# Kernel tuning notes

Hardware: AMD Instinct MI355X
Metric: run time of the kernel (lower is better)

The kernel has to match this reference:

```python
import jax, jax.numpy as jnp
import numpy as np

D_MODEL = 1024
NUM_HEADS = 16
D_K = D_MODEL // NUM_HEADS
ROPE_BASE = 10000.0


def _rope_cos_sin(seq_len, d_k):
    inv_freq = 1.0 / (ROPE_BASE ** (jnp.arange(0, d_k, 2, dtype=jnp.float32) / d_k))
    t = jnp.arange(seq_len, dtype=jnp.float32)
    freqs = t[:, None] * inv_freq[None, :]          # [S, d_k/2]
    emb = jnp.concatenate([freqs, freqs], axis=-1)  # [S, d_k]
    return jnp.cos(emb), jnp.sin(emb)


def _rotate_half(x):
    x1, x2 = jnp.split(x, 2, axis=-1)
    return jnp.concatenate([-x2, x1], axis=-1)


def setup_inputs() -> dict:
    key = jax.random.key(0)
    ks = jax.random.split(key, 11)
    B, S, D = 4, 2048, D_MODEL
    scale = 1.0 / np.sqrt(D)
    inp = {
        "query": jax.random.normal(ks[0], (B, S, D), jnp.float32),
        "key": jax.random.normal(ks[1], (B, S, D), jnp.float32),
        "value": jax.random.normal(ks[2], (B, S, D), jnp.float32),
        "W_q": jax.random.normal(ks[3], (D, D), jnp.float32) * scale,
        "b_q": jnp.zeros((D,), jnp.float32),
        "W_k": jax.random.normal(ks[4], (D, D), jnp.float32) * scale,
        "b_k": jnp.zeros((D,), jnp.float32),
        "W_v": jax.random.normal(ks[5], (D, D), jnp.float32) * scale,
        "b_v": jnp.zeros((D,), jnp.float32),
        "W_o": jax.random.normal(ks[6], (D, D), jnp.float32) * scale,
        "b_o": jnp.zeros((D,), jnp.float32),
    }
    return inp


def reference(query, key, value, W_q, b_q, W_k, b_k, W_v, b_v, W_o, b_o):
    B, Sq, D = query.shape
    Sk = key.shape[1]
    H, dk = NUM_HEADS, D_K

    # QKV projections -> [B, H, S, dk]
    Q = (query @ W_q.T + b_q).reshape(B, Sq, H, dk).transpose(0, 2, 1, 3)
    K = (key @ W_k.T + b_k).reshape(B, Sk, H, dk).transpose(0, 2, 1, 3)
    V = (value @ W_v.T + b_v).reshape(B, Sk, H, dk).transpose(0, 2, 1, 3)

    # RoPE
    cos, sin = _rope_cos_sin(Sq, dk)  # [S, dk]
    cos = cos[None, None]
    sin = sin[None, None]
    Q = Q * cos + _rotate_half(Q) * sin
    K = K * cos + _rotate_half(K) * sin

    scores = jnp.einsum("bhqd,bhkd->bhqk", Q, K) / np.sqrt(dk)
    causal_mask = jnp.triu(jnp.ones((Sq, Sk), bool), k=1)
    scores = jnp.where(causal_mask[None, None], -jnp.inf, scores)
    attn = jax.nn.softmax(scores, axis=-1)
    context = jnp.einsum("bhqk,bhkd->bhqd", attn, V)
    context = context.transpose(0, 2, 1, 3).reshape(B, Sq, D)
    return context @ W_o.T + b_o
```

## Files before the change

kernel.cpp:

```cpp
#include <hip/hip_runtime.h>
#include <hip/hip_bf16.h>
#include <cstdint>
#include <cstddef>


typedef __attribute__((ext_vector_type(8))) short short8;
typedef __attribute__((ext_vector_type(4))) float f32x4;
typedef unsigned short u16;

#define LOG2E 1.44269504088896340736f
#define SCALE_Q 0.18033688011112042f

__device__ __forceinline__ u16 f2bf(float f) {
  __hip_bfloat16 h = __float2bfloat16(f);
  return *reinterpret_cast<u16*>(&h);
}
__device__ __forceinline__ float bf2f(short bits) {
  unsigned int u = ((unsigned int)(u16)bits) << 16;
  return __uint_as_float(u);
}
__device__ __forceinline__ void gload_lds16(const void* g, void* l) {
  __builtin_amdgcn_global_load_lds(
      (const __attribute__((address_space(1))) void*)g,
      (__attribute__((address_space(3))) void*)l, 16, 0, 0);
}
__device__ __forceinline__ f32x4 max4(f32x4 a, f32x4 b) {
  f32x4 r;
  r[0] = fmaxf(a[0], b[0]); r[1] = fmaxf(a[1], b[1]);
  r[2] = fmaxf(a[2], b[2]); r[3] = fmaxf(a[3], b[3]);
  return r;
}

__global__ void cvt_f32_to_bf16(const float* __restrict__ in, u16* __restrict__ out, int n4) {
  const int stride = gridDim.x * blockDim.x;
  for (int i = blockIdx.x * blockDim.x + threadIdx.x; i < n4; i += stride) {
    const float4 v = ((const float4*)in)[i];
    ushort4 o;
    o.x = f2bf(v.x); o.y = f2bf(v.y); o.z = f2bf(v.z); o.w = f2bf(v.w);
    ((ushort4*)out)[i] = o;
  }
}

__global__ void rope_tables(float* __restrict__ cost, float* __restrict__ sint, int S) {
  const int idx = blockIdx.x * blockDim.x + threadIdx.x;
  if (idx >= S * 32) return;
  const int s = idx >> 5, i = idx & 31;
  const float invf = powf(10000.0f, -(float)i * (1.0f / 32.0f));
  const float ang = (float)s * invf;
  cost[idx] = cosf(ang);
  sint[idx] = sinf(ang);
}

template<int OUT_F32>
__global__ __launch_bounds__(256, 2)
void gemm_bt(const u16* __restrict__ A, const u16* __restrict__ Bt,
             const float* __restrict__ bias, void* __restrict__ Cout,
             int M, int N, int K) {
  __shared__ u16 As[128 * 64];
  __shared__ u16 Bs[128 * 64];
  const int tid = threadIdx.x;
  const int wid = tid >> 6;
  const int lane = tid & 63;
  const int g = lane >> 4, c = lane & 15;
  const int m0 = blockIdx.x * 128;
  const int n0 = blockIdx.y * 128;
  const int wr = wid >> 1, wc = wid & 1;

  f32x4 acc[4][4];
#pragma unroll
  for (int i = 0; i < 4; ++i)
#pragma unroll
    for (int j = 0; j < 4; ++j) acc[i][j] = (f32x4)(0.0f);

  const int kIters = K >> 6;
  for (int kt = 0; kt < kIters; ++kt) {
    const int k0 = kt << 6;
#pragma unroll
    for (int i = 0; i < 4; ++i) {
      const int chunk = i * 256 + tid;
      const int row = chunk >> 3;
      const int scz = (chunk & 7) ^ (row & 7);
      gload_lds16(A + (size_t)(m0 + row) * K + (k0 + scz * 8),
                  (char*)As + (size_t)(i * 256 + (wid << 6)) * 16);
      gload_lds16(Bt + (size_t)(n0 + row) * K + (k0 + scz * 8),
                  (char*)Bs + (size_t)(i * 256 + (wid << 6)) * 16);
    }
    __syncthreads();
#pragma unroll
    for (int ks = 0; ks < 2; ++ks) {
      short8 af[4], bfr[4];
#pragma unroll
      for (int mi = 0; mi < 4; ++mi) {
        const int row = wr * 64 + mi * 16 + c;
        const int cch = (g + ks * 4) ^ (row & 7);
        af[mi] = *(const short8*)((const char*)As + row * 128 + cch * 16);
      }
#pragma unroll
      for (int ni = 0; ni < 4; ++ni) {
        const int row = wc * 64 + ni * 16 + c;
        const int cch = (g + ks * 4) ^ (row & 7);
        bfr[ni] = *(const short8*)((const char*)Bs + row * 128 + cch * 16);
      }
#pragma unroll
      for (int mi = 0; mi < 4; ++mi)
#pragma unroll
        for (int ni = 0; ni < 4; ++ni)
          acc[mi][ni] = __builtin_amdgcn_mfma_f32_16x16x32_bf16(af[mi], bfr[ni], acc[mi][ni], 0, 0, 0);
    }
    __syncthreads();
  }

  float bv[4];
#pragma unroll
  for (int ni = 0; ni < 4; ++ni) bv[ni] = bias[n0 + wc * 64 + ni * 16 + c];

#pragma unroll
  for (int mi = 0; mi < 4; ++mi)
#pragma unroll
    for (int ni = 0; ni < 4; ++ni)
#pragma unroll
      for (int r = 0; r < 4; ++r) {
        const int row = m0 + wr * 64 + mi * 16 + g * 4 + r;
        const int col = n0 + wc * 64 + ni * 16 + c;
        const float v = acc[mi][ni][r] + bv[ni];
        if (OUT_F32) ((float*)Cout)[(size_t)row * N + col] = v;
        else         ((u16*)Cout)[(size_t)row * N + col] = f2bf(v);
      }
}

__global__ void reshape_rope(const u16* __restrict__ qp, const u16* __restrict__ kp,
                             const u16* __restrict__ vp,
                             const float* __restrict__ cost, const float* __restrict__ sint,
                             u16* __restrict__ Qh, u16* __restrict__ Kh, u16* __restrict__ Vtr,
                             int B, int H, int S) {
  __shared__ u16 tile[64][66];
  const int mode = blockIdx.z;
  const int bh = blockIdx.y;
  const int b = bh / H, h = bh % H;
  const int s0 = blockIdx.x * 64;
  const int t = threadIdx.x;
  const int D = H * 64;

  if (mode < 2) {
    const u16* src = mode ? kp : qp;
    u16* dst = mode ? Kh : Qh;
    const float qs = mode ? 1.0f : SCALE_Q;
    const int s = s0 + (t >> 2);
    const int dc = (t & 3) * 8;
    const u16* pr = src + (size_t)(b * S + s) * D + h * 64;
    const short8 lo = *(const short8*)(pr + dc);
    const short8 hi = *(const short8*)(pr + dc + 32);
    short8 olo, ohi;
#pragma unroll
    for (int j = 0; j < 8; ++j) {
      const float co = cost[s * 32 + dc + j];
      const float si = sint[s * 32 + dc + j];
      const float x1 = bf2f(lo[j]);
      const float x2 = bf2f(hi[j]);
      olo[j] = (short)f2bf((x1 * co - x2 * si) * qs);
      ohi[j] = (short)f2bf((x2 * co + x1 * si) * qs);
    }
    u16* op = dst + ((size_t)bh * S + s) * 64;
    *(short8*)(op + dc) = olo;
    *(short8*)(op + dc + 32) = ohi;
  } else {
#pragma unroll
    for (int it = 0; it < 2; ++it) {
      const int chunk = it * 256 + t;
      const int s = chunk >> 3;
      const int dc = (chunk & 7) * 8;
      const short8 v = *(const short8*)(vp + (size_t)(b * S + s0 + s) * D + h * 64 + dc);
#pragma unroll
      for (int u = 0; u < 8; ++u) tile[s][dc + u] = (u16)v[u];
    }
    __syncthreads();
    const int d = t >> 2;
    const int sc = (t & 3) * 16;
    u16* op = Vtr + ((size_t)bh * 64 + d) * S + s0 + sc;
    short8 v0, v1;
#pragma unroll
    for (int j = 0; j < 8; ++j) v0[j] = (short)tile[sc + j][d];
#pragma unroll
    for (int j = 0; j < 8; ++j) v1[j] = (short)tile[sc + 8 + j][d];
    *(short8*)op = v0;
    *(short8*)(op + 8) = v1;
  }
}

__global__ __launch_bounds__(256, 3)
void attn_kernel(const u16* __restrict__ Qh, const u16* __restrict__ Kh,
                 const u16* __restrict__ Vt, u16* __restrict__ ctx,
                 int B, int H, int S) {
  __shared__ u16 KV[2][2][64 * 64];
  __shared__ u16 Ps[4][16 * 64];
  const int tid = threadIdx.x, wid = tid >> 6, lane = tid & 63;
  const int g = lane >> 4, c = lane & 15;

  const int nstH = gridDim.x;
  const int nwg = nstH * gridDim.y;
  const int lin = blockIdx.x + nstH * blockIdx.y;
  const int tt = (lin & 7) * (nwg >> 3) + (lin >> 3);
  const int bx = tt % nstH;
  const int bh = tt / nstH;
  const int b = bh / H, h = bh % H;
  const int D = H * 64;
  const int NST = nstH * 2;

  const size_t baseQK = (size_t)bh * S * 64;
  const size_t baseV  = (size_t)bh * 64 * S;

  for (int ph = 0; ph < 2; ++ph) {
    const int stile = ph ? (NST - 1 - bx) : bx;
    const int q0 = stile * 128;
    const int KT = (q0 >> 6) + 2;
    const int q0w = q0 + wid * 32;
    const int ktl = (q0w + 31) >> 6;
    const int qg0 = q0w + c, qg1 = q0w + 16 + c;

    short8 qB[2][2];
#pragma unroll
    for (int qf = 0; qf < 2; ++qf)
#pragma unroll
      for (int ks = 0; ks < 2; ++ks)
        qB[qf][ks] = *(const short8*)(Qh + baseQK +
                       (size_t)(q0w + qf * 16 + c) * 64 + ks * 32 + g * 8);

    float m_r[2], l_r[2];
    m_r[0] = m_r[1] = -__builtin_inff();
    l_r[0] = l_r[1] = 0.0f;
    f32x4 o[4][2];
#pragma unroll
    for (int df = 0; df < 4; ++df) { o[df][0] = (f32x4)(0.0f); o[df][1] = (f32x4)(0.0f); }

    auto stage = [&](int buf, int kt) {
#pragma unroll
      for (int i = 0; i < 2; ++i) {
        const int chunk = i * 256 + tid;
        const int row = chunk >> 3;
        const int scz = (chunk & 7) ^ (row & 7);
        gload_lds16(Kh + baseQK + (size_t)(kt * 64 + row) * 64 + scz * 8,
                    (char*)&KV[buf][0][0] + (size_t)(i * 256 + (wid << 6)) * 16);
        gload_lds16(Vt + baseV + (size_t)row * S + (kt * 64 + scz * 8),
                    (char*)&KV[buf][1][0] + (size_t)(i * 256 + (wid << 6)) * 16);
      }
    };

    stage(0, 0);
    __syncthreads();
    int cur = 0;
    for (int kt = 0; kt < KT; ++kt) {
      if (kt + 1 < KT) stage(cur ^ 1, kt + 1);
      if (kt <= ktl) {
        const char* Kb = (const char*)&KV[cur][0][0];
        const char* Vb = (const char*)&KV[cur][1][0];

        f32x4 sc[4][2];
#pragma unroll
        for (int kf = 0; kf < 4; ++kf) { sc[kf][0] = (f32x4)(0.0f); sc[kf][1] = (f32x4)(0.0f); }
#pragma unroll
        for (int ks = 0; ks < 2; ++ks) {
          short8 kA[4];
#pragma unroll
          for (int kf = 0; kf < 4; ++kf) {
            const int row = kf * 16 + c;
            kA[kf] = *(const short8*)(Kb + row * 128 + (((g + 4 * ks) ^ (row & 7))) * 16);
          }
#pragma unroll
          for (int kf = 0; kf < 4; ++kf) {
            sc[kf][0] = __builtin_amdgcn_mfma_f32_16x16x32_bf16(kA[kf], qB[0][ks], sc[kf][0], 0, 0, 0);
            sc[kf][1] = __builtin_amdgcn_mfma_f32_16x16x32_bf16(kA[kf], qB[1][ks], sc[kf][1], 0, 0, 0);
          }
        }

        if (kt == ktl) {
#pragma unroll
          for (int kf = 0; kf < 4; ++kf)
#pragma unroll
            for (int r = 0; r < 4; ++r) {
              const int kg = kt * 64 + kf * 16 + 4 * g + r;
              if (kg > qg0) sc[kf][0][r] = -__builtin_inff();
              if (kg > qg1) sc[kf][1][r] = -__builtin_inff();
            }
        }

        u16* Pw = &Ps[wid][0];
        short8 pB[2][2];
#pragma unroll
        for (int qf = 0; qf < 2; ++qf) {
          f32x4 mm = max4(max4(sc[0][qf], sc[1][qf]), max4(sc[2][qf], sc[3][qf]));
          float pm = fmaxf(fmaxf(mm[0], mm[1]), fmaxf(mm[2], mm[3]));
          pm = fmaxf(pm, __shfl_xor(pm, 16));
          pm = fmaxf(pm, __shfl_xor(pm, 32));
          if (__any(pm > m_r[qf] + 8.0f)) {
            const float mn = fmaxf(m_r[qf], pm);
            const float rs = __builtin_exp2f(m_r[qf] - mn);
            m_r[qf] = mn; l_r[qf] *= rs;
#pragma unroll
            for (int df = 0; df < 4; ++df) o[df][qf] *= rs;
          }
          f32x4 ps4 = (f32x4)(0.0f);
#pragma unroll
          for (int kf = 0; kf < 4; ++kf) {
            f32x4 pv;
#pragma unroll
            for (int r = 0; r < 4; ++r) pv[r] = __builtin_exp2f(sc[kf][qf][r] - m_r[qf]);
            sc[kf][qf] = pv;
            ps4 += pv;
          }
          float psum = (ps4[0] + ps4[1]) + (ps4[2] + ps4[3]);
          psum += __shfl_xor(psum, 16);
          psum += __shfl_xor(psum, 32);
          l_r[qf] += psum;

#pragma unroll
          for (int kf = 0; kf < 4; ++kf) {
            ushort4 pk;
            pk.x = f2bf(sc[kf][qf][0]); pk.y = f2bf(sc[kf][qf][1]);
            pk.z = f2bf(sc[kf][qf][2]); pk.w = f2bf(sc[kf][qf][3]);
            *(ushort4*)((char*)Pw + c * 128 +
                        (((2 * kf + (g >> 1)) ^ (c & 7))) * 16 + 8 * (g & 1)) = pk;
          }
#pragma unroll
          for (int ks = 0; ks < 2; ++ks)
            pB[qf][ks] = *(const short8*)((const char*)Pw + c * 128 +
                                          (((g + 4 * ks) ^ (c & 7))) * 16);
        }

#pragma unroll
        for (int ks = 0; ks < 2; ++ks)
#pragma unroll
          for (int df = 0; df < 4; ++df) {
            const int row = df * 16 + c;
            const short8 va = *(const short8*)(Vb + row * 128 + (((g + 4 * ks) ^ (row & 7))) * 16);
            o[df][0] = __builtin_amdgcn_mfma_f32_16x16x32_bf16(va, pB[0][ks], o[df][0], 0, 0, 0);
            o[df][1] = __builtin_amdgcn_mfma_f32_16x16x32_bf16(va, pB[1][ks], o[df][1], 0, 0, 0);
          }
      }
      __syncthreads();
      cur ^= 1;
    }

#pragma unroll
    for (int qf = 0; qf < 2; ++qf) {
      const float inv = 1.0f / l_r[qf];
      u16* rowp = ctx + (size_t)(b * S + q0w + qf * 16 + c) * D + h * 64;
#pragma unroll
      for (int df = 0; df < 4; ++df) {
        ushort4 w;
        w.x = f2bf(o[df][qf][0] * inv); w.y = f2bf(o[df][qf][1] * inv);
        w.z = f2bf(o[df][qf][2] * inv); w.w = f2bf(o[df][qf][3] * inv);
        *(ushort4*)(rowp + df * 16 + 4 * g) = w;
      }
    }
  }
}

extern "C" void kernel_launch(void* const* d_in, const int* in_sizes, int n_in,
                              void* d_out, int out_size, void* d_ws, size_t ws_size,
                              hipStream_t stream) {
  const float* query = (const float*)d_in[0];
  const float* key   = (const float*)d_in[1];
  const float* value = (const float*)d_in[2];
  const float* W_q = (const float*)d_in[3];
  const float* b_q = (const float*)d_in[4];
  const float* W_k = (const float*)d_in[5];
  const float* b_k = (const float*)d_in[6];
  const float* W_v = (const float*)d_in[7];
  const float* b_v = (const float*)d_in[8];
  const float* W_o = (const float*)d_in[9];
  const float* b_o = (const float*)d_in[10];

  const int D = 1024, H = 16, S = 2048;
  const int BS = in_sizes[0] / D;
  const int B = BS / S;

  const size_t nX = (size_t)BS * D;
  const size_t nW = (size_t)D * D;
  u16* p = (u16*)d_ws;
  u16* xq = p;  p += nX;
  u16* xk = p;  p += nX;
  u16* xv = p;  p += nX;
  u16* wq = p;  p += nW;
  u16* wk = p;  p += nW;
  u16* wv = p;  p += nW;
  u16* wo = p;  p += nW;
  u16* qp = p;  p += nX;
  u16* kp = p;  p += nX;
  u16* vp = p;  p += nX;
  float* cost = (float*)p;
  float* sint = cost + (size_t)S * 32;
  u16* Qh = xq;
  u16* Kh = xk;
  u16* Vtr = xv;
  u16* ctx = qp;

  auto cvt = [&](const float* in, u16* out, size_t n) {
    int n4 = (int)(n / 4);
    int blocks = (n4 + 255) / 256; if (blocks > 2048) blocks = 2048;
    cvt_f32_to_bf16<<<blocks, 256, 0, stream>>>(in, out, n4);
  };
  cvt(query, xq, nX);
  cvt(key,   xk, nX);
  cvt(value, xv, nX);
  cvt(W_q, wq, nW);
  cvt(W_k, wk, nW);
  cvt(W_v, wv, nW);
  cvt(W_o, wo, nW);

  rope_tables<<<(S * 32 + 255) / 256, 256, 0, stream>>>(cost, sint, S);

  const dim3 gg(BS / 128, D / 128);
  gemm_bt<0><<<gg, 256, 0, stream>>>(xq, wq, b_q, qp, BS, D, D);
  gemm_bt<0><<<gg, 256, 0, stream>>>(xk, wk, b_k, kp, BS, D, D);
  gemm_bt<0><<<gg, 256, 0, stream>>>(xv, wv, b_v, vp, BS, D, D);

  reshape_rope<<<dim3(S / 64, B * H, 3), 256, 0, stream>>>(qp, kp, vp, cost, sint,
                                                           Qh, Kh, Vtr, B, H, S);

  attn_kernel<<<dim3(S / 256, B * H), 256, 0, stream>>>(Qh, Kh, Vtr, ctx, B, H, S);

  gemm_bt<1><<<gg, 256, 0, stream>>>(ctx, wo, b_o, d_out, BS, D, D);
}
```

Baseline: 363.3 us.

## Fuse RoPE and head reshape into projection GEMM epilogues, batch conversions

Moves the RoPE rotation, Q scaling, head-major reshape and V transpose into the epilogues of the QKV projection GEMMs, removing the separate reshape_rope kernel and its round trip through global memory. The seven fp32-to-bf16 conversion launches are merged into one kernel driven by a job table. GEMM blocks are remapped so that each XCD works on a contiguous range of M tiles. In exchange, the epilogue writes become scattered 2-byte and 8-byte stores, and it hardcodes S=2048 and H=16.

```diff
diff --git a/kernel.cpp b/kernel.cpp
--- a/kernel.cpp
+++ b/kernel.cpp
@@ -8,7 +8,6 @@
 typedef __attribute__((ext_vector_type(4))) float f32x4;
 typedef unsigned short u16;
 
-#define LOG2E 1.44269504088896340736f
 #define SCALE_Q 0.18033688011112042f
 
 __device__ __forceinline__ u16 f2bf(float f) {
@@ -31,13 +30,23 @@
   return r;
 }
 
-__global__ void cvt_f32_to_bf16(const float* __restrict__ in, u16* __restrict__ out, int n4) {
+struct CvtJobs {
+  const float* src[7];
+  u16* dst[7];
+  int pref[8];
+};
+
+__global__ void cvt_all(CvtJobs jobs, int total4) {
   const int stride = gridDim.x * blockDim.x;
-  for (int i = blockIdx.x * blockDim.x + threadIdx.x; i < n4; i += stride) {
-    const float4 v = ((const float4*)in)[i];
+  for (int i = blockIdx.x * blockDim.x + threadIdx.x; i < total4; i += stride) {
+    int j = 0;
+#pragma unroll
+    for (int t = 1; t < 7; ++t) j += (i >= jobs.pref[t]);
+    const int off = i - jobs.pref[j];
+    const float4 v = ((const float4*)jobs.src[j])[off];
     ushort4 o;
     o.x = f2bf(v.x); o.y = f2bf(v.y); o.z = f2bf(v.z); o.w = f2bf(v.w);
-    ((ushort4*)out)[i] = o;
+    ((ushort4*)jobs.dst[j])[off] = o;
   }
 }
 
@@ -51,19 +60,25 @@
   sint[idx] = sinf(ang);
 }
 
-template<int OUT_F32>
+template<int MODE>
 __global__ __launch_bounds__(256, 2)
-void gemm_bt(const u16* __restrict__ A, const u16* __restrict__ Bt,
-             const float* __restrict__ bias, void* __restrict__ Cout,
-             int M, int N, int K) {
+void gemm_fused(const u16* __restrict__ A, const u16* __restrict__ Bt,
+                const float* __restrict__ bias, void* __restrict__ Cout,
+                const float* __restrict__ cost, const float* __restrict__ sint,
+                int M, int N, int K, int S) {
   __shared__ u16 As[128 * 64];
   __shared__ u16 Bs[128 * 64];
   const int tid = threadIdx.x;
   const int wid = tid >> 6;
   const int lane = tid & 63;
   const int g = lane >> 4, c = lane & 15;
-  const int m0 = blockIdx.x * 128;
-  const int n0 = blockIdx.y * 128;
+
+  const int xcd = blockIdx.x & 7;
+  const int slot = blockIdx.x >> 3;
+  const int mPerX = (M >> 7) >> 3;
+  const int m0 = (xcd * mPerX + (slot % mPerX)) << 7;
+  const int n0 = (slot / mPerX) << 7;
+
   const int wr = wid >> 1, wc = wid & 1;
 
   f32x4 acc[4][4];
@@ -114,76 +129,61 @@
 #pragma unroll
   for (int ni = 0; ni < 4; ++ni) bv[ni] = bias[n0 + wc * 64 + ni * 16 + c];
 
-#pragma unroll
-  for (int mi = 0; mi < 4; ++mi)
-#pragma unroll
-    for (int ni = 0; ni < 4; ++ni)
-#pragma unroll
-      for (int r = 0; r < 4; ++r) {
-        const int row = m0 + wr * 64 + mi * 16 + g * 4 + r;
+  if (MODE == 3) {
+#pragma unroll
+    for (int mi = 0; mi < 4; ++mi)
+#pragma unroll
+      for (int ni = 0; ni < 4; ++ni)
+#pragma unroll
+        for (int r = 0; r < 4; ++r) {
+          const int row = m0 + wr * 64 + mi * 16 + g * 4 + r;
+          const int col = n0 + wc * 64 + ni * 16 + c;
+          ((float*)Cout)[(size_t)row * N + col] = acc[mi][ni][r] + bv[ni];
+        }
+  } else if (MODE == 2) {
+#pragma unroll
+    for (int mi = 0; mi < 4; ++mi) {
+      const int row_base = m0 + wr * 64 + mi * 16 + g * 4;
+      const int s = row_base & 2047;
+      const int b = row_base >> 11;
+#pragma unroll
+      for (int ni = 0; ni < 4; ++ni) {
         const int col = n0 + wc * 64 + ni * 16 + c;
-        const float v = acc[mi][ni][r] + bv[ni];
-        if (OUT_F32) ((float*)Cout)[(size_t)row * N + col] = v;
-        else         ((u16*)Cout)[(size_t)row * N + col] = f2bf(v);
-      }
-}
-
-__global__ void reshape_rope(const u16* __restrict__ qp, const u16* __restrict__ kp,
-                             const u16* __restrict__ vp,
-                             const float* __restrict__ cost, const float* __restrict__ sint,
-                             u16* __restrict__ Qh, u16* __restrict__ Kh, u16* __restrict__ Vtr,
-                             int B, int H, int S) {
-  __shared__ u16 tile[64][66];
-  const int mode = blockIdx.z;
-  const int bh = blockIdx.y;
-  const int b = bh / H, h = bh % H;
-  const int s0 = blockIdx.x * 64;
-  const int t = threadIdx.x;
-  const int D = H * 64;
-
-  if (mode < 2) {
-    const u16* src = mode ? kp : qp;
-    u16* dst = mode ? Kh : Qh;
-    const float qs = mode ? 1.0f : SCALE_Q;
-    const int s = s0 + (t >> 2);
-    const int dc = (t & 3) * 8;
-    const u16* pr = src + (size_t)(b * S + s) * D + h * 64;
-    const short8 lo = *(const short8*)(pr + dc);
-    const short8 hi = *(const short8*)(pr + dc + 32);
-    short8 olo, ohi;
-#pragma unroll
-    for (int j = 0; j < 8; ++j) {
-      const float co = cost[s * 32 + dc + j];
-      const float si = sint[s * 32 + dc + j];
-      const float x1 = bf2f(lo[j]);
-      const float x2 = bf2f(hi[j]);
-      olo[j] = (short)f2bf((x1 * co - x2 * si) * qs);
-      ohi[j] = (short)f2bf((x2 * co + x1 * si) * qs);
+        const int h = col >> 6;
+        const int d = ni * 16 + c;
+        ushort4 w;
+        w.x = f2bf(acc[mi][ni][0] + bv[ni]);
+        w.y = f2bf(acc[mi][ni][1] + bv[ni]);
+        w.z = f2bf(acc[mi][ni][2] + bv[ni]);
+        w.w = f2bf(acc[mi][ni][3] + bv[ni]);
+        *(ushort4*)((u16*)Cout + ((size_t)(b * 16 + h) * 64 + d) * (size_t)S + s) = w;
+      }
     }
-    u16* op = dst + ((size_t)bh * S + s) * 64;
-    *(short8*)(op + dc) = olo;
-    *(short8*)(op + dc + 32) = ohi;
   } else {
 #pragma unroll
-    for (int it = 0; it < 2; ++it) {
-      const int chunk = it * 256 + t;
-      const int s = chunk >> 3;
-      const int dc = (chunk & 7) * 8;
-      const short8 v = *(const short8*)(vp + (size_t)(b * S + s0 + s) * D + h * 64 + dc);
-#pragma unroll
-      for (int u = 0; u < 8; ++u) tile[s][dc + u] = (u16)v[u];
-    }
-    __syncthreads();
-    const int d = t >> 2;
-    const int sc = (t & 3) * 16;
-    u16* op = Vtr + ((size_t)bh * 64 + d) * S + s0 + sc;
-    short8 v0, v1;
-#pragma unroll
-    for (int j = 0; j < 8; ++j) v0[j] = (short)tile[sc + j][d];
-#pragma unroll
-    for (int j = 0; j < 8; ++j) v1[j] = (short)tile[sc + 8 + j][d];
-    *(short8*)op = v0;
-    *(short8*)(op + 8) = v1;
+    for (int mi = 0; mi < 4; ++mi)
+#pragma unroll
+      for (int pair = 0; pair < 2; ++pair) {
+        const int d_lo = pair * 16 + c;
+        const int col_lo = n0 + wc * 64 + d_lo;
+        const int h = col_lo >> 6;
+#pragma unroll
+        for (int r = 0; r < 4; ++r) {
+          const int row = m0 + wr * 64 + mi * 16 + g * 4 + r;
+          const int s = row & 2047;
+          const int b = row >> 11;
+          const float co = cost[s * 32 + d_lo];
+          const float si = sint[s * 32 + d_lo];
+          const float vlo = acc[mi][pair][r] + bv[pair];
+          const float vhi = acc[mi][pair + 2][r] + bv[pair + 2];
+          float olo = vlo * co - vhi * si;
+          float ohi = vhi * co + vlo * si;
+          if (MODE == 0) { olo *= SCALE_Q; ohi *= SCALE_Q; }
+          u16* dst = (u16*)Cout + ((size_t)(b * 16 + h) * S + s) * 64 + d_lo;
+          dst[0]  = f2bf(olo);
+          dst[32] = f2bf(ohi);
+        }
+      }
   }
 }
 
@@ -384,40 +384,33 @@
   u16* wk = p;  p += nW;
   u16* wv = p;  p += nW;
   u16* wo = p;  p += nW;
-  u16* qp = p;  p += nX;
-  u16* kp = p;  p += nX;
-  u16* vp = p;  p += nX;
+  u16* Qh = p;  p += nX;
+  u16* Kh = p;  p += nX;
+  u16* Vtr = p; p += nX;
   float* cost = (float*)p;
   float* sint = cost + (size_t)S * 32;
-  u16* Qh = xq;
-  u16* Kh = xk;
-  u16* Vtr = xv;
-  u16* ctx = qp;
-
-  auto cvt = [&](const float* in, u16* out, size_t n) {
-    int n4 = (int)(n / 4);
-    int blocks = (n4 + 255) / 256; if (blocks > 2048) blocks = 2048;
-    cvt_f32_to_bf16<<<blocks, 256, 0, stream>>>(in, out, n4);
-  };
-  cvt(query, xq, nX);
-  cvt(key,   xk, nX);
-  cvt(value, xv, nX);
-  cvt(W_q, wq, nW);
-  cvt(W_k, wk, nW);
-  cvt(W_v, wv, nW);
-  cvt(W_o, wo, nW);
+  u16* ctx = xq;
+
+  CvtJobs jobs;
+  jobs.src[0] = query; jobs.src[1] = key; jobs.src[2] = value;
+  jobs.src[3] = W_q;   jobs.src[4] = W_k; jobs.src[5] = W_v; jobs.src[6] = W_o;
+  jobs.dst[0] = xq; jobs.dst[1] = xk; jobs.dst[2] = xv;
+  jobs.dst[3] = wq; jobs.dst[4] = wk; jobs.dst[5] = wv; jobs.dst[6] = wo;
+  const int a4 = (int)(nX / 4), w4 = (int)(nW / 4);
+  jobs.pref[0] = 0;
+  jobs.pref[1] = a4;     jobs.pref[2] = 2 * a4; jobs.pref[3] = 3 * a4;
+  jobs.pref[4] = 3 * a4 + w4;     jobs.pref[5] = 3 * a4 + 2 * w4;
+  jobs.pref[6] = 3 * a4 + 3 * w4; jobs.pref[7] = 3 * a4 + 4 * w4;
+  cvt_all<<<2048, 256, 0, stream>>>(jobs, jobs.pref[7]);
 
   rope_tables<<<(S * 32 + 255) / 256, 256, 0, stream>>>(cost, sint, S);
 
-  const dim3 gg(BS / 128, D / 128);
-  gemm_bt<0><<<gg, 256, 0, stream>>>(xq, wq, b_q, qp, BS, D, D);
-  gemm_bt<0><<<gg, 256, 0, stream>>>(xk, wk, b_k, kp, BS, D, D);
-  gemm_bt<0><<<gg, 256, 0, stream>>>(xv, wv, b_v, vp, BS, D, D);
-
-  reshape_rope<<<dim3(S / 64, B * H, 3), 256, 0, stream>>>(qp, kp, vp, cost, sint,
-                                                           Qh, Kh, Vtr, B, H, S);
+  const int gblocks = (BS / 128) * (D / 128);
+  gemm_fused<0><<<gblocks, 256, 0, stream>>>(xq, wq, b_q, Qh,  cost, sint, BS, D, D, S);
+  gemm_fused<1><<<gblocks, 256, 0, stream>>>(xk, wk, b_k, Kh,  cost, sint, BS, D, D, S);
+  gemm_fused<2><<<gblocks, 256, 0, stream>>>(xv, wv, b_v, Vtr, cost, sint, BS, D, D, S);
 
   attn_kernel<<<dim3(S / 256, B * H), 256, 0, stream>>>(Qh, Kh, Vtr, ctx, B, H, S);
 
-  gemm_bt<1><<<gg, 256, 0, stream>>>(ctx, wo, b_o, d_out, BS, D, D);
-}
+  gemm_fused<3><<<gblocks, 256, 0, stream>>>(ctx, wo, b_o, d_out, cost, sint, BS, D, D, S);
+}
```

Result: faster. 334.1 us (-8.0%).
